# Optimization experiments

Measured on AMD Instinct MI355X. Metric: run time of the kernel, lower is better.

The kernel has to match this reference:

```python
import jax, jax.numpy as jnp
import numpy as np

RADIUS = 1.0
N_NORM = 1  # default n_norm in the torch module


def setup_inputs() -> dict:
    key = jax.random.key(0)
    k1, k2, k3 = jax.random.split(key, 3)
    batch, n, c_in, c_out = 8, 2048, 64, 64
    features = jax.random.normal(k1, (batch, n, c_in), dtype=jnp.float32)
    geometry = jax.random.normal(k2, (batch, n, 3), dtype=jnp.float32)
    # learned per-edge kernel weight: K(diff)[o,i] = sum_x diff[x] * Wk[x,o,i]
    Wk = jax.random.normal(k3, (3, c_out, c_in), dtype=jnp.float32) * 0.1
    return {"features": features, "geometry": geometry, "Wk": Wk}


def reference(features, geometry, Wk):
    # diff[z,a,b,:] = geometry[z,b] - geometry[z,a]   (rb - ra in the torch code)
    diff = geometry[:, None, :, :] - geometry[:, :, None, :]  # [z, a, b, 3]
    norm = jnp.sqrt(jnp.sum(diff * diff, axis=-1))            # [z, a, b]
    # Dense masked formulation: padding every point's neighbor list to k = n
    # with rel_mask zeros is mathematically identical to the torch variable-k
    # padding (masked entries contribute nothing to the einsum reduce).
    rel_mask = (norm < RADIUS).astype(features.dtype)         # [z, a, b]
    # Fused reduce. Original: einsum('zab,zabij,zabj->zai', mask, K(diff), feat[nei])
    # with K(diff)[z,a,b,i,j] = einsum('zabx,xij->zabij', diff, Wk). We contract
    # over b first to avoid materializing the [z,a,b,i,j] kernel tensor.
    s = jnp.einsum('zab,zabx,zbj->zaxj', rel_mask, diff, features)  # [z, a, 3, c_in]
    out = jnp.einsum('zaxj,xij->zai', s, Wk) / jnp.sqrt(jnp.asarray(N_NORM, features.dtype))
    return out
```

## Files before the change

### kernel.cpp

```cpp
#include <hip/hip_runtime.h>
#include <stdint.h>

#define NPTS 2048

#define BP_OFF    0ULL
#define BP_BYTES  (8ULL * 16 * 64 * 1024)
#define W2F_OFF   (BP_OFF + BP_BYTES)
#define W2F_BYTES (24ULL * 1024)
#define WXF_OFF   (W2F_OFF + W2F_BYTES)
#define WXF_BYTES (24ULL * 1024)

typedef __attribute__((ext_vector_type(8))) short bf16x8;
typedef __attribute__((ext_vector_type(4))) float f32x4;
typedef __attribute__((ext_vector_type(4))) unsigned int u32x4;

__device__ __forceinline__ unsigned f2bf(float f) {
  union { float f; unsigned u; } v; v.f = f;
  return (v.u + 0x7FFFu + ((v.u >> 16) & 1u)) >> 16;
}

__device__ __forceinline__ bf16x8 pack8(const float4 a, const float4 b) {
  u32x4 r;
  r[0] = f2bf(a.x) | (f2bf(a.y) << 16);
  r[1] = f2bf(a.z) | (f2bf(a.w) << 16);
  r[2] = f2bf(b.x) | (f2bf(b.y) << 16);
  r[3] = f2bf(b.z) | (f2bf(b.w) << 16);
  union { u32x4 u; bf16x8 h; } c; c.u = r; return c.h;
}

__global__ __launch_bounds__(256) void k1_prep(const float* __restrict__ feat,
                                               const float* __restrict__ geom,
                                               const float* __restrict__ Wk,
                                               unsigned char* __restrict__ ws) {
  const int blk = blockIdx.x, t = threadIdx.x;
  if (blk < 512) {
    const int z = blk >> 6, s = blk & 63;
    __shared__ __align__(16) float F[32][68];
    __shared__ float g[96];
    const float* fz = feat + ((size_t)z * NPTS + s * 32) * 64;
    {
      const int row = t >> 3, j0 = (t & 7) << 3;
      *(float4*)&F[row][j0]     = *(const float4*)&fz[row * 64 + j0];
      *(float4*)&F[row][j0 + 4] = *(const float4*)&fz[row * 64 + j0 + 4];
    }
    if (t < 96) g[t] = geom[((size_t)z * NPTS + s * 32) * 3 + t];
    __syncthreads();
    const int q = t, x = q >> 6, j = q & 63, qb = q >> 4, nn = q & 15;
    unsigned char* dst = ws + BP_OFF + (((size_t)z * 16 + qb) * 64 + s) * 1024 + nn * 64;
#pragma unroll
    for (int quad = 0; quad < 4; ++quad) {
      u32x4 pv;
#pragma unroll
      for (int p = 0; p < 4; ++p) {
        const int k0 = quad * 8 + 2 * p;
        float f0 = F[k0][j], f1 = F[k0 + 1][j];
        if (x < 3) { f0 *= g[k0 * 3 + x]; f1 *= g[(k0 + 1) * 3 + x]; }
        pv[p] = f2bf(f0) | (f2bf(f1) << 16);
      }
      *(u32x4*)(dst + quad * 16) = pv;
    }
  } else if (blk == 512) {
    for (int e = t; e < 1536; e += 256) {
      const int frag = e >> 6, lp = e & 63, nn = lp >> 2, qd = lp & 3;
      const int kb = frag >> 2, cb = frag & 3;
      u32x4 pv;
#pragma unroll
      for (int p = 0; p < 4; ++p) {
        const int k0 = kb * 32 + qd * 8 + 2 * p;
        const float v0 = Wk[(k0 >> 6) * 4096 + (cb * 16 + nn) * 64 + (k0 & 63)];
        const float v1 = Wk[((k0 + 1) >> 6) * 4096 + (cb * 16 + nn) * 64 + ((k0 + 1) & 63)];
        pv[p] = f2bf(v0) | (f2bf(v1) << 16);
      }
      *(u32x4*)(ws + W2F_OFF + (size_t)frag * 1024 + lp * 16) = pv;
    }
  } else {
    for (int e = t; e < 1536; e += 256) {
      const int frag = e >> 6, lp = e & 63, nn = lp >> 2, qd = lp & 3;
      const int kb = frag / 12, cb = frag % 12, xi = cb * 16 + nn;
      u32x4 pv;
#pragma unroll
      for (int p = 0; p < 4; ++p) {
        const int k0 = kb * 32 + qd * 8 + 2 * p;
        const float v0 = Wk[(xi >> 6) * 4096 + (xi & 63) * 64 + k0];
        const float v1 = Wk[(xi >> 6) * 4096 + (xi & 63) * 64 + k0 + 1];
        pv[p] = f2bf(v0) | (f2bf(v1) << 16);
      }
      *(u32x4*)(ws + WXF_OFF + (size_t)frag * 1024 + lp * 16) = pv;
    }
  }
}

__global__ __launch_bounds__(512, 2) void k2_fused(const float* __restrict__ geom,
                                                   const unsigned char* __restrict__ ws,
                                                   float* __restrict__ out) {
  __shared__ __align__(16) float glds[NPTS * 3];
  __shared__ unsigned int Mw[64 * 64];
  __shared__ __align__(16) float Ct[32 * 256];

  const int t = threadIdx.x, lane = t & 63, w = t >> 6;
  const int quad = lane >> 4, n = lane & 15;
  const int z = blockIdx.x >> 5, a0 = (blockIdx.x & 31) * 64;

  const float* gz = geom + (size_t)z * NPTS * 3;
#pragma unroll
  for (int i = 0; i < 3; ++i) {
    const int idx = (i * 512 + t) * 4;
    *(float4*)&glds[idx] = *(const float4*)&gz[idx];
  }
  __syncthreads();

  {
    const int mr = t & 63, sg = t >> 6;
    const float pa0 = glds[(a0 + mr) * 3 + 0];
    const float pa1 = glds[(a0 + mr) * 3 + 1];
    const float pa2 = glds[(a0 + mr) * 3 + 2];
#pragma unroll
    for (int si = 0; si < 8; ++si) {
      const int s = sg * 8 + si;
      unsigned bits = 0;
#pragma unroll
      for (int k8 = 0; k8 < 4; ++k8) {
        float v[24];
#pragma unroll
        for (int i = 0; i < 6; ++i)
          *(float4*)&v[i * 4] = *(const float4*)&glds[s * 96 + k8 * 24 + i * 4];
#pragma unroll
        for (int p = 0; p < 8; ++p) {
          const float d0 = v[p * 3 + 0] - pa0;
          const float d1 = v[p * 3 + 1] - pa1;
          const float d2 = v[p * 3 + 2] - pa2;
          const float n2 = fmaf(d2, d2, fmaf(d1, d1, d0 * d0));
          bits |= (n2 < 1.0f ? 1u : 0u) << (k8 * 8 + p);
        }
      }
      Mw[s * 64 + mr] = bits;
    }
  }
  __syncthreads();

  const unsigned char* bpz = ws + BP_OFF + (size_t)z * 16 * 65536;
  const int fragoff = n * 64 + quad * 16;
  const int qsh = quad * 8;

  f32x4 acc[4][2];
#pragma unroll
  for (int rb = 0; rb < 4; ++rb)
#pragma unroll
    for (int cb = 0; cb < 2; ++cb)
#pragma unroll
      for (int r = 0; r < 4; ++r) acc[rb][cb][r] = 0.f;

  bf16x8 B0[2], B1[2];
#pragma unroll
  for (int cb = 0; cb < 2; ++cb) {
    B0[cb] = *(const bf16x8*)(bpz + ((size_t)(2 * w + cb) * 64 + 0) * 1024 + fragoff);
    B1[cb] = *(const bf16x8*)(bpz + ((size_t)(2 * w + cb) * 64 + 1) * 1024 + fragoff);
  }

#define UNPACK_MFMA(SS, BB)                                                       \
  {                                                                               \
    unsigned mb[4];                                                               \
    _Pragma("unroll") for (int rb = 0; rb < 4; ++rb)                              \
        mb[rb] = Mw[(SS) * 64 + rb * 16 + n];                                     \
    _Pragma("unroll") for (int rb = 0; rb < 4; ++rb) {                            \
      const unsigned mq = mb[rb] >> qsh;                                          \
      u32x4 aw;                                                                   \
      _Pragma("unroll") for (int tt = 0; tt < 4; ++tt)                            \
          aw[tt] = ((mq >> (2 * tt)) & 1u) * 0x3F80u |                            \
                   ((mq >> (2 * tt + 1)) & 1u) * 0x3F800000u;                     \
      union { u32x4 u; bf16x8 h; } cv; cv.u = aw;                                 \
      _Pragma("unroll") for (int cb = 0; cb < 2; ++cb)                            \
        acc[rb][cb] = __builtin_amdgcn_mfma_f32_16x16x32_bf16(                    \
            cv.h, BB[cb], acc[rb][cb], 0, 0, 0);                                  \
    }                                                                             \
  }

  for (int s2 = 0; s2 < 64; s2 += 2) {
    UNPACK_MFMA(s2, B0)
    {
      const int sl = (s2 + 2) > 63 ? 63 : (s2 + 2);
#pragma unroll
      for (int cb = 0; cb < 2; ++cb)
        B0[cb] = *(const bf16x8*)(bpz + ((size_t)(2 * w + cb) * 64 + sl) * 1024 + fragoff);
    }
    UNPACK_MFMA(s2 + 1, B1)
    {
      const int sl = (s2 + 3) > 63 ? 63 : (s2 + 3);
#pragma unroll
      for (int cb = 0; cb < 2; ++cb)
        B1[cb] = *(const bf16x8*)(bpz + ((size_t)(2 * w + cb) * 64 + sl) * 1024 + fragoff);
    }
  }
#undef UNPACK_MFMA

  bf16x8 Across[8];
#pragma unroll
  for (int p = 0; p < 2; ++p) {
#pragma unroll
    for (int rb2 = 0; rb2 < 2; ++rb2)
#pragma unroll
      for (int cb = 0; cb < 2; ++cb)
#pragma unroll
        for (int r = 0; r < 4; ++r) {
          const int lm = rb2 * 16 + quad * 4 + r;
          const int col = 32 * w + cb * 16 + n;
          Ct[lm * 256 + (((col >> 2) ^ lm) << 2) + (col & 3)] = acc[2 * p + rb2][cb][r];
        }
    __syncthreads();
    if ((w >> 1) == p) {
      const int lm = 16 * (w & 1) + n;
#pragma unroll
      for (int kb = 0; kb < 8; ++kb) {
        const int c0 = (kb * 8 + quad * 2) ^ lm;
        const int c1 = (kb * 8 + quad * 2 + 1) ^ lm;
        const float4 f0 = *(const float4*)&Ct[lm * 256 + (c0 << 2)];
        const float4 f1 = *(const float4*)&Ct[lm * 256 + (c1 << 2)];
        Across[kb] = pack8(f0, f1);
      }
    }
    __syncthreads();
  }

  if (w < 4) {
    f32x4 mn[4], V[12];
#pragma unroll
    for (int i = 0; i < 4; ++i)
#pragma unroll
      for (int r = 0; r < 4; ++r) mn[i][r] = 0.f;
#pragma unroll
    for (int i = 0; i < 12; ++i)
#pragma unroll
      for (int r = 0; r < 4; ++r) V[i][r] = 0.f;

    const unsigned char* w2f = ws + W2F_OFF;
    const unsigned char* wxf = ws + WXF_OFF;
#pragma unroll
    for (int kb = 0; kb < 6; ++kb)
#pragma unroll
      for (int cb = 0; cb < 4; ++cb) {
        const bf16x8 Bf = *(const bf16x8*)(w2f + (size_t)(kb * 4 + cb) * 1024 + fragoff);
        mn[cb] = __builtin_amdgcn_mfma_f32_16x16x32_bf16(Across[kb], Bf, mn[cb], 0, 0, 0);
      }
#pragma unroll
    for (int kb = 0; kb < 2; ++kb)
#pragma unroll
      for (int cb = 0; cb < 12; ++cb) {
        const bf16x8 Bf = *(const bf16x8*)(wxf + (size_t)(kb * 12 + cb) * 1024 + fragoff);
        V[cb] = __builtin_amdgcn_mfma_f32_16x16x32_bf16(Across[6 + kb], Bf, V[cb], 0, 0, 0);
      }

#pragma unroll
    for (int r = 0; r < 4; ++r) {
      const int af = a0 + 16 * w + quad * 4 + r;
      const float g0 = glds[af * 3 + 0], g1 = glds[af * 3 + 1], g2 = glds[af * 3 + 2];
#pragma unroll
      for (int cb = 0; cb < 4; ++cb) {
        const float v = mn[cb][r] - g0 * V[cb][r] - g1 * V[cb + 4][r] - g2 * V[cb + 8][r];
        out[((size_t)z * NPTS + af) * 64 + cb * 16 + n] = v;
      }
    }
  }
}

extern "C" void kernel_launch(void* const* d_in, const int* in_sizes, int n_in,
                              void* d_out, int out_size, void* d_ws, size_t ws_size,
                              hipStream_t stream) {
  const float* feat = (const float*)d_in[0];
  const float* geom = (const float*)d_in[1];
  const float* Wk   = (const float*)d_in[2];
  float* out = (float*)d_out;
  unsigned char* ws = (unsigned char*)d_ws;

  k1_prep<<<dim3(514), 256, 0, stream>>>(feat, geom, Wk, ws);
  k2_fused<<<dim3(256), 512, 0, stream>>>(geom, ws, out);
}
```

Measured before the change: 109.8 us.

## Remap MFMA warp tiling to share mask unpack across eight column blocks

The main masked-sum loop changes its wave tiling. Each wave now owns one 16-row block and eight 16-column blocks instead of four row blocks by two column blocks, so each mask word is unpacked once per step and feeds eight MFMAs, with a cheaper bit-to-bf16 expansion. This holds more B fragments in registers (16 bf16x8), and the LDS transpose buffer doubles so the reduction runs in one pass with a single barrier. The prep kernel now transposes features through LDS so its workspace stores are lane-contiguous, and blocks are reordered to interleave batches across the grid.

```diff
diff --git a/kernel.cpp b/kernel.cpp
--- a/kernel.cpp
+++ b/kernel.cpp
@@ -35,29 +35,45 @@
   const int blk = blockIdx.x, t = threadIdx.x;
   if (blk < 512) {
     const int z = blk >> 6, s = blk & 63;
-    __shared__ __align__(16) float F[32][68];
+    __shared__ float FT[64][37];
     __shared__ float g[96];
     const float* fz = feat + ((size_t)z * NPTS + s * 32) * 64;
     {
       const int row = t >> 3, j0 = (t & 7) << 3;
-      *(float4*)&F[row][j0]     = *(const float4*)&fz[row * 64 + j0];
-      *(float4*)&F[row][j0 + 4] = *(const float4*)&fz[row * 64 + j0 + 4];
+      const float4 v0 = *(const float4*)&fz[row * 64 + j0];
+      const float4 v1 = *(const float4*)&fz[row * 64 + j0 + 4];
+      FT[j0 + 0][row] = v0.x; FT[j0 + 1][row] = v0.y;
+      FT[j0 + 2][row] = v0.z; FT[j0 + 3][row] = v0.w;
+      FT[j0 + 4][row] = v1.x; FT[j0 + 5][row] = v1.y;
+      FT[j0 + 6][row] = v1.z; FT[j0 + 7][row] = v1.w;
     }
     if (t < 96) g[t] = geom[((size_t)z * NPTS + s * 32) * 3 + t];
     __syncthreads();
-    const int q = t, x = q >> 6, j = q & 63, qb = q >> 4, nn = q & 15;
-    unsigned char* dst = ws + BP_OFF + (((size_t)z * 16 + qb) * 64 + s) * 1024 + nn * 64;
-#pragma unroll
-    for (int quad = 0; quad < 4; ++quad) {
+
+    const int w = t >> 6, L = t & 63;
+    const int n = L >> 2, k0 = (L & 3) * 8;
+    const int j = w * 16 + n;
+    float f[8];
+#pragma unroll
+    for (int i = 0; i < 8; ++i) f[i] = FT[j][k0 + i];
+    float gx[3][8];
+#pragma unroll
+    for (int x = 0; x < 3; ++x)
+#pragma unroll
+      for (int i = 0; i < 8; ++i) gx[x][i] = g[(k0 + i) * 3 + x];
+
+    unsigned char* base = ws + BP_OFF + (size_t)z * 1048576 + (size_t)w * 65536 +
+                          (size_t)s * 1024 + L * 16;
+#pragma unroll
+    for (int it = 0; it < 4; ++it) {
       u32x4 pv;
 #pragma unroll
       for (int p = 0; p < 4; ++p) {
-        const int k0 = quad * 8 + 2 * p;
-        float f0 = F[k0][j], f1 = F[k0 + 1][j];
-        if (x < 3) { f0 *= g[k0 * 3 + x]; f1 *= g[(k0 + 1) * 3 + x]; }
+        float f0 = f[2 * p], f1 = f[2 * p + 1];
+        if (it < 3) { f0 *= gx[it][2 * p]; f1 *= gx[it][2 * p + 1]; }
         pv[p] = f2bf(f0) | (f2bf(f1) << 16);
       }
-      *(u32x4*)(dst + quad * 16) = pv;
+      *(u32x4*)(base + (size_t)it * 4 * 65536) = pv;
     }
   } else if (blk == 512) {
     for (int e = t; e < 1536; e += 256) {
@@ -95,11 +111,11 @@
                                                    float* __restrict__ out) {
   __shared__ __align__(16) float glds[NPTS * 3];
   __shared__ unsigned int Mw[64 * 64];
-  __shared__ __align__(16) float Ct[32 * 256];
+  __shared__ __align__(16) float Ct[64 * 256];
 
   const int t = threadIdx.x, lane = t & 63, w = t >> 6;
   const int quad = lane >> 4, n = lane & 15;
-  const int z = blockIdx.x >> 5, a0 = (blockIdx.x & 31) * 64;
+  const int z = blockIdx.x & 7, a0 = ((blockIdx.x >> 3) & 31) * 64;
 
   const float* gz = geom + (size_t)z * NPTS * 3;
 #pragma unroll
@@ -138,90 +154,71 @@
   }
   __syncthreads();
 
-  const unsigned char* bpz = ws + BP_OFF + (size_t)z * 16 * 65536;
+  const unsigned char* bpz = ws + BP_OFF + (size_t)z * 1048576;
   const int fragoff = n * 64 + quad * 16;
   const int qsh = quad * 8;
-
-  f32x4 acc[4][2];
-#pragma unroll
-  for (int rb = 0; rb < 4; ++rb)
-#pragma unroll
-    for (int cb = 0; cb < 2; ++cb)
-#pragma unroll
-      for (int r = 0; r < 4; ++r) acc[rb][cb][r] = 0.f;
-
-  bf16x8 B0[2], B1[2];
-#pragma unroll
-  for (int cb = 0; cb < 2; ++cb) {
-    B0[cb] = *(const bf16x8*)(bpz + ((size_t)(2 * w + cb) * 64 + 0) * 1024 + fragoff);
-    B1[cb] = *(const bf16x8*)(bpz + ((size_t)(2 * w + cb) * 64 + 1) * 1024 + fragoff);
-  }
-
-#define UNPACK_MFMA(SS, BB)                                                       \
+  const int rbase = 16 * (w & 3);
+  const int qb0 = 8 * (w >> 2);
+
+  f32x4 acc[8];
+#pragma unroll
+  for (int cb = 0; cb < 8; ++cb)
+#pragma unroll
+    for (int r = 0; r < 4; ++r) acc[cb][r] = 0.f;
+
+  bf16x8 Bf0[8], Bf1[8];
+#pragma unroll
+  for (int cb = 0; cb < 8; ++cb) {
+    Bf0[cb] = *(const bf16x8*)(bpz + (size_t)(qb0 + cb) * 65536 + 0 * 1024 + fragoff);
+    Bf1[cb] = *(const bf16x8*)(bpz + (size_t)(qb0 + cb) * 65536 + 1 * 1024 + fragoff);
+  }
+
+#define STEP(SS, BB)                                                              \
   {                                                                               \
-    unsigned mb[4];                                                               \
-    _Pragma("unroll") for (int rb = 0; rb < 4; ++rb)                              \
-        mb[rb] = Mw[(SS) * 64 + rb * 16 + n];                                     \
-    _Pragma("unroll") for (int rb = 0; rb < 4; ++rb) {                            \
-      const unsigned mq = mb[rb] >> qsh;                                          \
-      u32x4 aw;                                                                   \
-      _Pragma("unroll") for (int tt = 0; tt < 4; ++tt)                            \
-          aw[tt] = ((mq >> (2 * tt)) & 1u) * 0x3F80u |                            \
-                   ((mq >> (2 * tt + 1)) & 1u) * 0x3F800000u;                     \
-      union { u32x4 u; bf16x8 h; } cv; cv.u = aw;                                 \
-      _Pragma("unroll") for (int cb = 0; cb < 2; ++cb)                            \
-        acc[rb][cb] = __builtin_amdgcn_mfma_f32_16x16x32_bf16(                    \
-            cv.h, BB[cb], acc[rb][cb], 0, 0, 0);                                  \
-    }                                                                             \
+    const unsigned mq = Mw[(SS) * 64 + rbase + n] >> qsh;                         \
+    u32x4 aw;                                                                     \
+    aw[0] = (mq & 1u)   * 0x3F80u | (mq & 2u)   * 0x1FC00000u;                    \
+    aw[1] = (mq & 4u)   * 0x0FE0u | (mq & 8u)   * 0x07F00000u;                    \
+    aw[2] = (mq & 16u)  * 0x03F8u | (mq & 32u)  * 0x01FC0000u;                    \
+    aw[3] = (mq & 64u)  * 0xFEu   | (mq & 128u) * 0x007F0000u;                    \
+    union { u32x4 u; bf16x8 h; } cv; cv.u = aw;                                   \
+    _Pragma("unroll") for (int cb = 0; cb < 8; ++cb)                              \
+      acc[cb] = __builtin_amdgcn_mfma_f32_16x16x32_bf16(cv.h, BB[cb],             \
+                                                        acc[cb], 0, 0, 0);        \
+    const int sl = ((SS) + 2) > 63 ? 63 : ((SS) + 2);                             \
+    _Pragma("unroll") for (int cb = 0; cb < 8; ++cb)                              \
+      BB[cb] = *(const bf16x8*)(bpz + (size_t)(qb0 + cb) * 65536 +                \
+                                (size_t)sl * 1024 + fragoff);                     \
   }
 
   for (int s2 = 0; s2 < 64; s2 += 2) {
-    UNPACK_MFMA(s2, B0)
-    {
-      const int sl = (s2 + 2) > 63 ? 63 : (s2 + 2);
-#pragma unroll
-      for (int cb = 0; cb < 2; ++cb)
-        B0[cb] = *(const bf16x8*)(bpz + ((size_t)(2 * w + cb) * 64 + sl) * 1024 + fragoff);
-    }
-    UNPACK_MFMA(s2 + 1, B1)
-    {
-      const int sl = (s2 + 3) > 63 ? 63 : (s2 + 3);
-#pragma unroll
-      for (int cb = 0; cb < 2; ++cb)
-        B1[cb] = *(const bf16x8*)(bpz + ((size_t)(2 * w + cb) * 64 + sl) * 1024 + fragoff);
-    }
-  }
-#undef UNPACK_MFMA
-
-  bf16x8 Across[8];
-#pragma unroll
-  for (int p = 0; p < 2; ++p) {
-#pragma unroll
-    for (int rb2 = 0; rb2 < 2; ++rb2)
-#pragma unroll
-      for (int cb = 0; cb < 2; ++cb)
-#pragma unroll
-        for (int r = 0; r < 4; ++r) {
-          const int lm = rb2 * 16 + quad * 4 + r;
-          const int col = 32 * w + cb * 16 + n;
-          Ct[lm * 256 + (((col >> 2) ^ lm) << 2) + (col & 3)] = acc[2 * p + rb2][cb][r];
-        }
-    __syncthreads();
-    if ((w >> 1) == p) {
-      const int lm = 16 * (w & 1) + n;
-#pragma unroll
-      for (int kb = 0; kb < 8; ++kb) {
-        const int c0 = (kb * 8 + quad * 2) ^ lm;
-        const int c1 = (kb * 8 + quad * 2 + 1) ^ lm;
-        const float4 f0 = *(const float4*)&Ct[lm * 256 + (c0 << 2)];
-        const float4 f1 = *(const float4*)&Ct[lm * 256 + (c1 << 2)];
-        Across[kb] = pack8(f0, f1);
-      }
-    }
-    __syncthreads();
-  }
+    STEP(s2, Bf0)
+    STEP(s2 + 1, Bf1)
+  }
+#undef STEP
+
+#pragma unroll
+  for (int cb = 0; cb < 8; ++cb)
+#pragma unroll
+    for (int r = 0; r < 4; ++r) {
+      const int row = rbase + quad * 4 + r;
+      const int col = (qb0 + cb) * 16 + n;
+      Ct[row * 256 + (((col >> 2) ^ row) << 2) + (col & 3)] = acc[cb][r];
+    }
+  __syncthreads();
 
   if (w < 4) {
+    const int lm = 16 * w + n;
+    bf16x8 Across[8];
+#pragma unroll
+    for (int kb = 0; kb < 8; ++kb) {
+      const int c0 = (kb * 8 + quad * 2) ^ lm;
+      const int c1 = (kb * 8 + quad * 2 + 1) ^ lm;
+      const float4 f0 = *(const float4*)&Ct[lm * 256 + c0 * 4];
+      const float4 f1 = *(const float4*)&Ct[lm * 256 + c1 * 4];
+      Across[kb] = pack8(f0, f1);
+    }
+
     f32x4 mn[4], V[12];
 #pragma unroll
     for (int i = 0; i < 4; ++i)
@@ -238,15 +235,15 @@
     for (int kb = 0; kb < 6; ++kb)
 #pragma unroll
       for (int cb = 0; cb < 4; ++cb) {
-        const bf16x8 Bf = *(const bf16x8*)(w2f + (size_t)(kb * 4 + cb) * 1024 + fragoff);
-        mn[cb] = __builtin_amdgcn_mfma_f32_16x16x32_bf16(Across[kb], Bf, mn[cb], 0, 0, 0);
+        const bf16x8 Bfr = *(const bf16x8*)(w2f + (size_t)(kb * 4 + cb) * 1024 + fragoff);
+        mn[cb] = __builtin_amdgcn_mfma_f32_16x16x32_bf16(Across[kb], Bfr, mn[cb], 0, 0, 0);
       }
 #pragma unroll
     for (int kb = 0; kb < 2; ++kb)
 #pragma unroll
       for (int cb = 0; cb < 12; ++cb) {
-        const bf16x8 Bf = *(const bf16x8*)(wxf + (size_t)(kb * 12 + cb) * 1024 + fragoff);
-        V[cb] = __builtin_amdgcn_mfma_f32_16x16x32_bf16(Across[6 + kb], Bf, V[cb], 0, 0, 0);
+        const bf16x8 Bfr = *(const bf16x8*)(wxf + (size_t)(kb * 12 + cb) * 1024 + fragoff);
+        V[cb] = __builtin_amdgcn_mfma_f32_16x16x32_bf16(Across[6 + kb], Bfr, V[cb], 0, 0, 0);
       }
 
 #pragma unroll
```

Result: slower. 139.7 us (+27.3%).
